# Kernel optimization log

Hardware: AMD Instinct MI355X
Metric: run time of the kernel (lower is better)

Reference implementation:

```python
import jax, jax.numpy as jnp
import numpy as np

B, S, D = 4, 2048, 1024
H, DH = 16, 64
THETA = 10000.0


def _rope_tables(seq_len, dim):
    # freqs_cis = exp(i * t * f), here as cos/sin tables, shape [S, dim//2]
    freqs = 1.0 / (THETA ** (jnp.arange(0, dim, 2, dtype=jnp.float32) / dim))
    ang = jnp.outer(jnp.arange(seq_len, dtype=jnp.float32), freqs)
    return jnp.cos(ang), jnp.sin(ang)


def _apply_rope(x, cos, sin):
    # x: [B,S,H,DH]; pairs are interleaved (x[...,2i], x[...,2i+1])
    xe = x[..., 0::2]
    xo = x[..., 1::2]
    c = cos[None, :, None, :]
    s = sin[None, :, None, :]
    out = jnp.stack([xe * c - xo * s, xe * s + xo * c], axis=-1)
    return out.reshape(x.shape).astype(x.dtype)


def setup_inputs() -> dict:
    key = jax.random.key(0)
    ks = jax.random.split(key, 5)
    x = jax.random.normal(ks[0], (B, S, D), dtype=jnp.float32)
    Wq = jax.random.normal(ks[1], (D, D), dtype=jnp.float32) * 0.02
    Wk = jax.random.normal(ks[2], (D, D), dtype=jnp.float32) * 0.02
    Wv = jax.random.normal(ks[3], (D, D), dtype=jnp.float32) * 0.02
    Wo = jax.random.normal(ks[4], (D, D), dtype=jnp.float32) * 0.02
    lambdas = jnp.zeros((2,), dtype=jnp.float32)
    return {"x": x, "Wq": Wq, "Wk": Wk, "Wv": Wv, "Wo": Wo, "lambdas": lambdas}


def reference(x, Wq, Wk, Wv, Wo, lambdas):
    scale = 1.0 / np.sqrt(DH)
    q = (x @ Wq.T).reshape(B, S, H, DH)
    k = (x @ Wk.T).reshape(B, S, H, DH)
    v = (x @ Wv.T).reshape(B, S, H, DH)
    cos, sin = _rope_tables(S, DH)
    q = _apply_rope(q, cos, sin)
    k = _apply_rope(k, cos, sin)
    # explicit QK^T with causal mask, softmax, then @V (dropout is identity in eval)
    attn = jnp.einsum('bshd,bthd->bhst', q, k) * scale  # [B,H,S,S]
    causal = jnp.tril(jnp.ones((S, S), dtype=bool))
    attn = jnp.where(causal[None, None], attn, -jnp.inf)
    probs = jax.nn.softmax(attn, axis=-1)
    head_out = jnp.einsum('bhst,bthd->bshd', probs, v)  # [B,S,H,DH]
    out = head_out.reshape(B, S, D) @ Wo.T
    return out
```

## Files before the change

### kernel.cpp

```cpp
#include <hip/hip_runtime.h>
#include <math.h>

static constexpr int Bsz = 4, Sq = 2048, Dm = 1024, NH = 16, DHd = 64;
static constexpr int Mrows = Bsz * Sq;
static constexpr float ROPE_LN = 0.14391156831212787f;
static constexpr float QSCALE = 0.18033688011112043f;

typedef _Float16 half8 __attribute__((ext_vector_type(8)));
typedef _Float16 half4v __attribute__((ext_vector_type(4)));
typedef __fp16 fp16x2 __attribute__((ext_vector_type(2)));
typedef float f32x4 __attribute__((ext_vector_type(4)));

__device__ __forceinline__ void gl_lds16(const void* g, void* l) {
    __builtin_amdgcn_global_load_lds(
        (const __attribute__((address_space(1))) void*)g,
        (__attribute__((address_space(3))) void*)l, 16, 0, 0);
}

__device__ __forceinline__ float exp2_hw(float x) {
    float r;
    asm volatile("v_exp_f32 %0, %1" : "=v"(r) : "v"(x));
    return r;
}

__global__ __launch_bounds__(256) void prep_kernel(
    const float* __restrict__ x,
    const float* __restrict__ Wq, const float* __restrict__ Wk,
    const float* __restrict__ Wv, const float* __restrict__ Wo,
    _Float16* __restrict__ xh,
    _Float16* __restrict__ Wqh, _Float16* __restrict__ Wkh,
    _Float16* __restrict__ Wvh, _Float16* __restrict__ Woh,
    float2* __restrict__ rope)
{
    const int i = blockIdx.x * 256 + threadIdx.x;
    if (i < 2097152) {
        const float4 v = ((const float4*)x)[i];
        half4v hv;
        hv[0] = (_Float16)v.x; hv[1] = (_Float16)v.y;
        hv[2] = (_Float16)v.z; hv[3] = (_Float16)v.w;
        ((half4v*)xh)[i] = hv;
    } else if (i < 3145728) {
        const int w = (i - 2097152) >> 18;
        const int off = (i - 2097152) & 262143;
        const float* s = (w == 0) ? Wq : (w == 1) ? Wk : (w == 2) ? Wv : Wo;
        _Float16* d = (w == 0) ? Wqh : (w == 1) ? Wkh : (w == 2) ? Wvh : Woh;
        const float sc = (w == 0) ? QSCALE : 1.0f;
        const float4 v = ((const float4*)s)[off];
        half4v hv;
        hv[0] = (_Float16)(v.x * sc); hv[1] = (_Float16)(v.y * sc);
        hv[2] = (_Float16)(v.z * sc); hv[3] = (_Float16)(v.w * sc);
        ((half4v*)d)[off] = hv;
    } else {
        const int t = i - 3145728;
        const int pos = t >> 5, j = t & 31;
        const float f = expf(-ROPE_LN * (float)(2 * j));
        const float a = (float)pos * f;
        rope[t] = make_float2(cosf(a), sinf(a));
    }
}

template <typename OutT, int MODE>
__device__ __forceinline__ void mfma_gemm_body(
    const _Float16* __restrict__ A, const _Float16* __restrict__ W,
    OutT* __restrict__ C, const float2* __restrict__ rope, int K, int N,
    int m0, int n0)
{
    __shared__ _Float16 As[2][128 * 32];
    __shared__ _Float16 Bs[2][128 * 32];

    const int tid = threadIdx.x;
    const int wave = tid >> 6, lane = tid & 63;
    const int quad = lane >> 4, l16 = lane & 15;
    const int wm = (wave >> 1) * 64, wn = (wave & 1) * 64;

    const _Float16* gA[2]; const _Float16* gB[2];
    int lOff[2];
    #pragma unroll
    for (int i = 0; i < 2; ++i) {
        const int F = (wave * 2 + i) * 64 + lane;
        const int r = F >> 2, cp = F & 3;
        const int c = cp ^ ((r >> 1) & 3);
        gA[i] = A + (size_t)(m0 + r) * K + c * 8;
        gB[i] = W + (size_t)(n0 + r) * K + c * 8;
        lOff[i] = (wave * 2 + i) * 512;
    }

    const int sw = (l16 >> 1) & 3;
    int offA[4], offB[4];
    #pragma unroll
    for (int t = 0; t < 4; ++t) {
        offA[t] = (wm + t * 16 + l16) * 32 + ((quad ^ sw) * 8);
        offB[t] = (wn + t * 16 + l16) * 32 + ((quad ^ sw) * 8);
    }

    f32x4 acc[4][4];
    #pragma unroll
    for (int im = 0; im < 4; ++im)
        #pragma unroll
        for (int nb = 0; nb < 4; ++nb)
            #pragma unroll
            for (int r = 0; r < 4; ++r) acc[im][nb][r] = 0.f;

    for (int k0 = 0; k0 < K; k0 += 64) {
        __syncthreads();
        #pragma unroll
        for (int kh = 0; kh < 2; ++kh)
            #pragma unroll
            for (int i = 0; i < 2; ++i) {
                gl_lds16(gA[i] + k0 + kh * 32, &As[kh][lOff[i]]);
                gl_lds16(gB[i] + k0 + kh * 32, &Bs[kh][lOff[i]]);
            }
        __syncthreads();

        #pragma unroll
        for (int kh = 0; kh < 2; ++kh) {
            half8 a[4], b[4];
            #pragma unroll
            for (int t = 0; t < 4; ++t) {
                a[t] = *(const half8*)&As[kh][offA[t]];
                b[t] = *(const half8*)&Bs[kh][offB[t]];
            }
            #pragma unroll
            for (int im = 0; im < 4; ++im)
                #pragma unroll
                for (int nb = 0; nb < 4; ++nb)
                    acc[im][nb] = __builtin_amdgcn_mfma_f32_16x16x32_f16(
                        a[im], b[nb], acc[im][nb], 0, 0, 0);
        }
    }

    #pragma unroll
    for (int nb = 0; nb < 4; ++nb) {
        const int n = n0 + wn + nb * 16 + l16;
        if constexpr (MODE == 2) {
            const int hb = ((m0 + wm) >> 11) * 16 + (n >> 6);
            const int dh = n & 63;
            const int tb = (m0 + wm) & (Sq - 1);
            half8 v0, v1;
            #pragma unroll
            for (int r = 0; r < 4; ++r)
                #pragma unroll
                for (int im = 0; im < 4; ++im) {
                    const int idx = r * 4 + im;
                    const _Float16 h = (_Float16)acc[im][nb][r];
                    if (idx < 8) v0[idx] = h; else v1[idx - 8] = h;
                }
            _Float16* dst = C + (((size_t)hb * 64 + dh) << 11) + tb + quad * 16;
            *(half8*)dst = v0;
            *(half8*)(dst + 8) = v1;
        } else {
            const int j = (n & 63) >> 1;
            #pragma unroll
            for (int im = 0; im < 4; ++im) {
                #pragma unroll
                for (int r = 0; r < 4; ++r) {
                    const int m = m0 + wm + im * 16 + quad * 4 + r;
                    float v = acc[im][nb][r];
                    if constexpr (MODE == 1) {
                        const int pos = m & (Sq - 1);
                        const float2 cs = rope[pos * 32 + j];
                        const float vp = __shfl_xor(v, 1);
                        v = (n & 1) ? (vp * cs.y + v * cs.x)
                                    : (v * cs.x - vp * cs.y);
                        C[(size_t)m * N + n] = (_Float16)v;
                    } else {
                        C[(size_t)m * N + n] = v;
                    }
                }
            }
        }
    }
}

__device__ __forceinline__ void xcd_swizzle(int& m0, int& n0) {
    const int orig = blockIdx.x + (blockIdx.y << 3);
    const int xcd = orig & 7, j = orig >> 3;
    m0 = (xcd * 8 + (j >> 3)) * 128;
    n0 = (j & 7) * 128;
}

__global__ __launch_bounds__(256) void qkv_mfma_kernel(
    const _Float16* __restrict__ xh,
    const _Float16* __restrict__ Wq, const _Float16* __restrict__ Wk,
    const _Float16* __restrict__ Wv,
    _Float16* __restrict__ Qo, _Float16* __restrict__ Ko,
    _Float16* __restrict__ VTp, const float2* __restrict__ rope)
{
    int m0, n0;
    xcd_swizzle(m0, n0);
    const int z = blockIdx.z;
    if (z == 0)
        mfma_gemm_body<_Float16, 1>(xh, Wq, Qo, rope, Dm, Dm, m0, n0);
    else if (z == 1)
        mfma_gemm_body<_Float16, 1>(xh, Wk, Ko, rope, Dm, Dm, m0, n0);
    else
        mfma_gemm_body<_Float16, 2>(xh, Wv, VTp, nullptr, Dm, Dm, m0, n0);
}

__global__ __launch_bounds__(256) void oproj_mfma_kernel(
    const _Float16* __restrict__ HOh, const _Float16* __restrict__ Wo,
    float* __restrict__ out)
{
    int m0, n0;
    xcd_swizzle(m0, n0);
    mfma_gemm_body<float, 0>(HOh, Wo, out, nullptr, Dm, Dm, m0, n0);
}

__global__ __launch_bounds__(256) void attn_mfma_kernel(
    const _Float16* __restrict__ Q, const _Float16* __restrict__ K,
    const _Float16* __restrict__ VT, _Float16* __restrict__ HO)
{
    __shared__ _Float16 Ks[64 * 64];
    __shared__ _Float16 Vs[64 * 64];
    __shared__ _Float16 Ps[4][32][72];

    const int tid = threadIdx.x;
    const int wave = tid >> 6, lane = tid & 63;
    const int quad = lane >> 4, l16 = lane & 15;
    const int id = blockIdx.x;
    const int hb = id & 63;
    const int qi = 15 - (id >> 6);
    const int h = hb & 15, b = hb >> 4;
    const int q0 = qi * 128;
    const size_t base = (size_t)b * Sq * Dm + (size_t)h * DHd;
    const size_t vtbase = (size_t)hb * 64 * Sq;

    half8 ones;
    #pragma unroll
    for (int i = 0; i < 8; ++i) ones[i] = (_Float16)1.0f;

    half8 aQ[2][2];
    #pragma unroll
    for (int mf = 0; mf < 2; ++mf) {
        const _Float16* qrow =
            Q + base + (size_t)(q0 + wave * 32 + mf * 16 + l16) * Dm + quad * 8;
        aQ[mf][0] = *(const half8*)(qrow);
        aQ[mf][1] = *(const half8*)(qrow + 32);
    }

    f32x4 Oacc[2][4];
    #pragma unroll
    for (int mf = 0; mf < 2; ++mf)
        #pragma unroll
        for (int nb = 0; nb < 4; ++nb)
            #pragma unroll
            for (int r = 0; r < 4; ++r) Oacc[mf][nb][r] = 0.f;
    f32x4 lacc[2];
    #pragma unroll
    for (int mf = 0; mf < 2; ++mf)
        #pragma unroll
        for (int r = 0; r < 4; ++r) lacc[mf][r] = 0.f;

    auto stage_tile = [&](int t0) {
        #pragma unroll
        for (int i = 0; i < 2; ++i) {
            const int F = (wave * 2 + i) * 64 + lane;
            const int r = F >> 3;
            const int cl = (F & 7) ^ (r & 7);
            gl_lds16(K + base + (size_t)(t0 + r) * Dm + cl * 8,
                     &Ks[(wave * 2 + i) * 512]);
            gl_lds16(VT + vtbase + ((size_t)r << 11) + t0 + cl * 8,
                     &Vs[(wave * 2 + i) * 512]);
        }
    };

    auto do_tile = [&](int dd, bool diag) {
        f32x4 sacc[2][4];
        #pragma unroll
        for (int mf = 0; mf < 2; ++mf)
            #pragma unroll
            for (int nb = 0; nb < 4; ++nb)
                #pragma unroll
                for (int r = 0; r < 4; ++r) sacc[mf][nb][r] = 0.f;
        __builtin_amdgcn_s_setprio(1);
        #pragma unroll
        for (int kstep = 0; kstep < 2; ++kstep) {
            #pragma unroll
            for (int nb = 0; nb < 4; ++nb) {
                const int krow = nb * 16 + l16;
                const int kch = (kstep * 4 + quad) ^ (krow & 7);
                const half8 bK = *(const half8*)&Ks[krow * 64 + kch * 8];
                #pragma unroll
                for (int mf = 0; mf < 2; ++mf)
                    sacc[mf][nb] = __builtin_amdgcn_mfma_f32_16x16x32_f16(
                        aQ[mf][kstep], bK, sacc[mf][nb], 0, 0, 0);
            }
        }
        __builtin_amdgcn_s_setprio(0);

        #pragma unroll
        for (int mf = 0; mf < 2; ++mf)
            #pragma unroll
            for (int r = 0; r < 4; ++r) {
                float e[4];
                #pragma unroll
                for (int nb = 0; nb < 4; ++nb) {
                    float v = sacc[mf][nb][r];
                    if (diag && (nb * 16 + l16 + dd >
                                 wave * 32 + mf * 16 + quad * 4 + r))
                        v = -1.0e4f;
                    e[nb] = exp2_hw(v);
                }
                const fp16x2 lo = __builtin_amdgcn_cvt_pkrtz(e[0], e[1]);
                const fp16x2 hi = __builtin_amdgcn_cvt_pkrtz(e[2], e[3]);
                uint2 pk;
                pk.x = __builtin_bit_cast(unsigned int, lo);
                pk.y = __builtin_bit_cast(unsigned int, hi);
                *(uint2*)&Ps[wave][mf * 16 + quad * 4 + r][l16 * 4] = pk;
            }

        __builtin_amdgcn_s_setprio(1);
        #pragma unroll
        for (int kstep = 0; kstep < 2; ++kstep) {
            half8 aP[2];
            #pragma unroll
            for (int mf = 0; mf < 2; ++mf) {
                aP[mf] = *(const half8*)
                    &Ps[wave][mf * 16 + l16][kstep * 32 + quad * 8];
                lacc[mf] = __builtin_amdgcn_mfma_f32_16x16x32_f16(
                    aP[mf], ones, lacc[mf], 0, 0, 0);
            }
            #pragma unroll
            for (int nb = 0; nb < 4; ++nb) {
                const int vrow = nb * 16 + l16;
                const int vch = (kstep * 4 + quad) ^ (vrow & 7);
                const half8 bV = *(const half8*)&Vs[vrow * 64 + vch * 8];
                #pragma unroll
                for (int mf = 0; mf < 2; ++mf)
                    Oacc[mf][nb] = __builtin_amdgcn_mfma_f32_16x16x32_f16(
                        aP[mf], bV, Oacc[mf][nb], 0, 0, 0);
            }
        }
        __builtin_amdgcn_s_setprio(0);
    };

    const int nt = 2 * qi + 2;
    for (int t = 0; t < nt; ++t) {
        __syncthreads();
        stage_tile(t * 64);
        __syncthreads();
        do_tile(t * 64 - q0, t >= nt - 2);
    }

    #pragma unroll
    for (int mf = 0; mf < 2; ++mf) {
        float inv[4];
        #pragma unroll
        for (int r = 0; r < 4; ++r) inv[r] = 1.0f / lacc[mf][r];
        #pragma unroll
        for (int nb = 0; nb < 4; ++nb)
            #pragma unroll
            for (int r = 0; r < 4; ++r) {
                const int row = wave * 32 + mf * 16 + quad * 4 + r;
                HO[base + (size_t)(q0 + row) * Dm + nb * 16 + l16] =
                    (_Float16)(Oacc[mf][nb][r] * inv[r]);
            }
    }
}

extern "C" void kernel_launch(void* const* d_in, const int* in_sizes, int n_in,
                              void* d_out, int out_size, void* d_ws, size_t ws_size,
                              hipStream_t stream)
{
    const float* x  = (const float*)d_in[0];
    const float* Wq = (const float*)d_in[1];
    const float* Wk = (const float*)d_in[2];
    const float* Wv = (const float*)d_in[3];
    const float* Wo = (const float*)d_in[4];
    float* out = (float*)d_out;

    const size_t matX = (size_t)Mrows * Dm;
    const size_t matW = (size_t)Dm * Dm;

    _Float16* xh  = (_Float16*)d_ws;
    _Float16* Wqh = xh + matX;
    _Float16* Wkh = Wqh + matW;
    _Float16* Wvh = Wkh + matW;
    _Float16* Woh = Wvh + matW;
    _Float16* Qh  = Woh + matW;
    _Float16* Kh  = Qh + matX;
    _Float16* VTp = Kh + matX;
    _Float16* HOh = VTp + matX;
    float2* rope  = (float2*)(HOh + matX);

    dim3 blk(256);
    prep_kernel<<<(3145728 + 65536) / 256, blk, 0, stream>>>(
        x, Wq, Wk, Wv, Wo, xh, Wqh, Wkh, Wvh, Woh, rope);
    qkv_mfma_kernel<<<dim3(Dm / 128, Mrows / 128, 3), blk, 0, stream>>>(
        xh, Wqh, Wkh, Wvh, Qh, Kh, VTp, rope);
    attn_mfma_kernel<<<dim3(16 * NH * Bsz), blk, 0, stream>>>(
        Qh, Kh, VTp, HOh);
    oproj_mfma_kernel<<<dim3(Dm / 128, Mrows / 128, 1), blk, 0, stream>>>(
        HOh, Woh, out);
}
```

Measured before the change: 248.5 us.

## Load K/V fragments directly from global memory instead of staging through LDS

The attention kernel stops staging K and V tiles into shared memory with two block barriers per tile. Each wave now reads its MFMA B-operand fragments for K and V^T straight from global memory (relying on L1/L2 reuse across the four waves), and launch bounds ask for four blocks per CU. This removes the LDS staging cost and the __syncthreads stalls. In exchange every wave issues its own global loads, which multiplies traffic through the cache by four and exposes global latency with no explicit prefetch.

```diff
diff --git a/kernel.cpp b/kernel.cpp
--- a/kernel.cpp
+++ b/kernel.cpp
@@ -206,12 +206,10 @@
     mfma_gemm_body<float, 0>(HOh, Wo, out, nullptr, Dm, Dm, m0, n0);
 }
 
-__global__ __launch_bounds__(256) void attn_mfma_kernel(
+__global__ __launch_bounds__(256, 4) void attn_mfma_kernel(
     const _Float16* __restrict__ Q, const _Float16* __restrict__ K,
     const _Float16* __restrict__ VT, _Float16* __restrict__ HO)
 {
-    __shared__ _Float16 Ks[64 * 64];
-    __shared__ _Float16 Vs[64 * 64];
     __shared__ _Float16 Ps[4][32][72];
 
     const int tid = threadIdx.x;
@@ -251,20 +249,10 @@
         #pragma unroll
         for (int r = 0; r < 4; ++r) lacc[mf][r] = 0.f;
 
-    auto stage_tile = [&](int t0) {
-        #pragma unroll
-        for (int i = 0; i < 2; ++i) {
-            const int F = (wave * 2 + i) * 64 + lane;
-            const int r = F >> 3;
-            const int cl = (F & 7) ^ (r & 7);
-            gl_lds16(K + base + (size_t)(t0 + r) * Dm + cl * 8,
-                     &Ks[(wave * 2 + i) * 512]);
-            gl_lds16(VT + vtbase + ((size_t)r << 11) + t0 + cl * 8,
-                     &Vs[(wave * 2 + i) * 512]);
-        }
-    };
-
-    auto do_tile = [&](int dd, bool diag) {
+    auto do_tile = [&](int t0, int dd, bool diag) {
+        const _Float16* Kt = K + base + (size_t)t0 * Dm;
+        const _Float16* Vt = VT + vtbase + t0;
+
         f32x4 sacc[2][4];
         #pragma unroll
         for (int mf = 0; mf < 2; ++mf)
@@ -272,21 +260,22 @@
             for (int nb = 0; nb < 4; ++nb)
                 #pragma unroll
                 for (int r = 0; r < 4; ++r) sacc[mf][nb][r] = 0.f;
-        __builtin_amdgcn_s_setprio(1);
         #pragma unroll
         for (int kstep = 0; kstep < 2; ++kstep) {
-            #pragma unroll
-            for (int nb = 0; nb < 4; ++nb) {
-                const int krow = nb * 16 + l16;
-                const int kch = (kstep * 4 + quad) ^ (krow & 7);
-                const half8 bK = *(const half8*)&Ks[krow * 64 + kch * 8];
+            half8 bK[4];
+            #pragma unroll
+            for (int nb = 0; nb < 4; ++nb)
+                bK[nb] = *(const half8*)&Kt[(size_t)(nb * 16 + l16) * Dm +
+                                            (kstep * 4 + quad) * 8];
+            __builtin_amdgcn_s_setprio(1);
+            #pragma unroll
+            for (int nb = 0; nb < 4; ++nb)
                 #pragma unroll
                 for (int mf = 0; mf < 2; ++mf)
                     sacc[mf][nb] = __builtin_amdgcn_mfma_f32_16x16x32_f16(
-                        aQ[mf][kstep], bK, sacc[mf][nb], 0, 0, 0);
-            }
+                        aQ[mf][kstep], bK[nb], sacc[mf][nb], 0, 0, 0);
+            __builtin_amdgcn_s_setprio(0);
         }
-        __builtin_amdgcn_s_setprio(0);
 
         #pragma unroll
         for (int mf = 0; mf < 2; ++mf)
@@ -309,38 +298,36 @@
                 *(uint2*)&Ps[wave][mf * 16 + quad * 4 + r][l16 * 4] = pk;
             }
 
-        __builtin_amdgcn_s_setprio(1);
         #pragma unroll
         for (int kstep = 0; kstep < 2; ++kstep) {
+            half8 bV[4];
+            #pragma unroll
+            for (int nb = 0; nb < 4; ++nb)
+                bV[nb] = *(const half8*)&Vt[((size_t)(nb * 16 + l16) << 11) +
+                                            (kstep * 4 + quad) * 8];
             half8 aP[2];
             #pragma unroll
-            for (int mf = 0; mf < 2; ++mf) {
+            for (int mf = 0; mf < 2; ++mf)
                 aP[mf] = *(const half8*)
                     &Ps[wave][mf * 16 + l16][kstep * 32 + quad * 8];
+            __builtin_amdgcn_s_setprio(1);
+            #pragma unroll
+            for (int mf = 0; mf < 2; ++mf)
                 lacc[mf] = __builtin_amdgcn_mfma_f32_16x16x32_f16(
                     aP[mf], ones, lacc[mf], 0, 0, 0);
-            }
-            #pragma unroll
-            for (int nb = 0; nb < 4; ++nb) {
-                const int vrow = nb * 16 + l16;
-                const int vch = (kstep * 4 + quad) ^ (vrow & 7);
-                const half8 bV = *(const half8*)&Vs[vrow * 64 + vch * 8];
+            #pragma unroll
+            for (int nb = 0; nb < 4; ++nb)
                 #pragma unroll
                 for (int mf = 0; mf < 2; ++mf)
                     Oacc[mf][nb] = __builtin_amdgcn_mfma_f32_16x16x32_f16(
-                        aP[mf], bV, Oacc[mf][nb], 0, 0, 0);
-            }
+                        aP[mf], bV[nb], Oacc[mf][nb], 0, 0, 0);
+            __builtin_amdgcn_s_setprio(0);
         }
-        __builtin_amdgcn_s_setprio(0);
     };
 
     const int nt = 2 * qi + 2;
-    for (int t = 0; t < nt; ++t) {
-        __syncthreads();
-        stage_tile(t * 64);
-        __syncthreads();
-        do_tile(t * 64 - q0, t >= nt - 2);
-    }
+    for (int t = 0; t < nt; ++t)
+        do_tile(t * 64, t * 64 - q0, t >= nt - 2);
 
     #pragma unroll
     for (int mf = 0; mf < 2; ++mf) {
```

New measurement: 392.1 us. +57.8%, slower.
